# Performance work log

Hardware: AMD Instinct MI355X
Metric: run time of the kernel (lower is better)

## Reference

```python
import jax, jax.numpy as jnp
import numpy as np

N_E = 8192
E_DIM = 64
BETA = 0.25
DIVERSITY_GAMMA = 1.0
INV_TEMP = 100.0
EPS = 1e-05


def _entropy(p):
    # matches torch: (-p * log(clamp(p, min=eps))).sum(-1)
    return (-p * jnp.log(jnp.clip(p, EPS))).sum(axis=-1)


def setup_inputs() -> dict:
    key = jax.random.key(0)
    k1, k2 = jax.random.split(key)
    z = jax.random.normal(k1, (16, E_DIM, 32, 32), dtype=jnp.float32)
    # codebook, init like nn.Embedding then uniform_(-1/n_e, 1/n_e) scale doesn't matter for math;
    # use a small uniform init faithful to the module
    emb = jax.random.uniform(k2, (N_E, E_DIM), dtype=jnp.float32,
                             minval=-1.0 / N_E, maxval=1.0 / N_E)
    return {"z": z, "emb": emb}


def reference(z, emb):
    sg = jax.lax.stop_gradient
    # b c h w -> b h w c
    zp = jnp.transpose(z, (0, 2, 3, 1))            # [B,H,W,C]
    zf = zp.reshape(-1, E_DIM)                      # [N, C]
    # pairwise squared distances: ||z||^2 + ||e||^2 - 2 z e^T
    d = (jnp.sum(zf * zf, axis=1, keepdims=True)
         + jnp.sum(emb * emb, axis=1)
         - 2.0 * jnp.einsum('nd,kd->nk', zf, emb))  # [N, n_e]
    min_indices = jnp.argmin(d, axis=1)             # [N]
    z_q = emb[min_indices].reshape(zp.shape)        # gather, [B,H,W,C]
    # legacy commitment loss
    loss = (jnp.mean((sg(z_q) - zp) ** 2)
            + BETA * jnp.mean((z_q - sg(zp)) ** 2))
    # entropy aux loss (frac_per_sample_entropy == 1.0)
    prob = jax.nn.softmax(-d * INV_TEMP, axis=-1)   # [N, n_e]
    per_sample_entropy = _entropy(prob).mean()
    avg_prob = prob.mean(axis=0)                    # [n_e]
    codebook_entropy = _entropy(avg_prob)
    entropy_aux = per_sample_entropy - DIVERSITY_GAMMA * codebook_entropy
    # straight-through estimator
    z_q = zp + sg(z_q - zp)
    quantized = jnp.transpose(z_q, (0, 3, 1, 2))    # b h w c -> b c h w
    return quantized, loss, entropy_aux, min_indices
```

## Files before the change

kernel.cpp:

```cpp
#include <hip/hip_runtime.h>
#include <cfloat>


typedef __attribute__((ext_vector_type(8))) short short8v;
typedef __attribute__((ext_vector_type(4))) float f32x4;

#define C100L2E 144.26950408889634f
#define C200L2E 288.53900817779268f
#define LN2 0.6931471805599453

#define BLOB_TILE 33792
#define OFF_BLOB   0
#define OFF_INVZ   2162688
#define OFF_MINIDX 2228224
#define OFF_AVG    2293760
#define OFF_PSE    2326528
#define OFF_ZPART  2326544
#define OFF_S1PART (OFF_ZPART + 262144)
#define OFF_DMPART (OFF_S1PART + 262144)
#define OFF_IMPART (OFF_DMPART + 262144)
#define OFF_LOSSP  (OFF_IMPART + 262144)
#define OFF_ZZ     (OFF_LOSSP + 32768)

__device__ __forceinline__ unsigned short f2bf_rne(float f) {
    unsigned u = __float_as_uint(f);
    u = (u + 0x7fffu + ((u >> 16) & 1u)) >> 16;
    return (unsigned short)u;
}

__device__ __forceinline__ void gload_lds16(const void* g, void* l) {
    __builtin_amdgcn_global_load_lds(
        (const __attribute__((address_space(1))) unsigned int*)g,
        (__attribute__((address_space(3))) unsigned int*)l, 16, 0, 0);
}

__global__ __launch_bounds__(256) void k_prep(
    const float* __restrict__ emb, const float* __restrict__ z,
    char* __restrict__ blob, char* __restrict__ zblob, float* __restrict__ zz)
{
    if (blockIdx.x < 32) {
        const int k = blockIdx.x * 256 + threadIdx.x;
        const float* row = emb + k * 64;
        float fv[64];
#pragma unroll
        for (int i = 0; i < 16; ++i) {
            float4 v = ((const float4*)row)[i];
            fv[4 * i] = v.x; fv[4 * i + 1] = v.y; fv[4 * i + 2] = v.z; fv[4 * i + 3] = v.w;
        }
        float r8[8];
#pragma unroll
        for (int j = 0; j < 8; ++j) r8[j] = __fmul_rn(fv[j], fv[j]);
#pragma unroll
        for (int i = 8; i < 64; i += 8)
#pragma unroll
            for (int j = 0; j < 8; ++j)
                r8[j] = __fadd_rn(r8[j], __fmul_rn(fv[i + j], fv[i + j]));
        float s01 = __fadd_rn(r8[0], r8[1]), s23 = __fadd_rn(r8[2], r8[3]);
        float s45 = __fadd_rn(r8[4], r8[5]), s67 = __fadd_rn(r8[6], r8[7]);
        float e2 = __fadd_rn(__fadd_rn(s01, s23), __fadd_rn(s45, s67));

        char* tb = blob + (size_t)(k >> 7) * BLOB_TILE;
        const int r = k & 127;
        ((float*)(tb + 32768))[r] = e2;
        ((float*)(tb + 33280))[r] = e2 * C100L2E;
        const int sw = (r & 7) << 4;
#pragma unroll
        for (int dh = 0; dh < 2; ++dh)
#pragma unroll
            for (int cg = 0; cg < 4; ++cg) {
                short8v hv, lv;
#pragma unroll
                for (int e = 0; e < 8; ++e) {
                    float f = fv[dh * 32 + cg * 8 + e];
                    unsigned short hb = f2bf_rne(f);
                    float hf = __uint_as_float((unsigned)hb << 16);
                    hv[e] = (short)hb;
                    lv[e] = (short)f2bf_rne(f - hf);
                }
                const int byt = (r * 128 + dh * 64 + cg * 16) ^ sw;
                *(short8v*)(tb + byt) = hv;
                *(short8v*)(tb + 16384 + byt) = lv;
            }
    } else {
        const int r = (blockIdx.x - 32) * 256 + threadIdx.x;
        const float* src = z + (r >> 10) * 65536 + (r & 1023);
        float fv[64];
#pragma unroll
        for (int c = 0; c < 64; ++c) fv[c] = src[c * 1024];

        float r8[8];
#pragma unroll
        for (int j = 0; j < 8; ++j) r8[j] = __fmul_rn(fv[j], fv[j]);
#pragma unroll
        for (int i = 8; i < 64; i += 8)
#pragma unroll
            for (int j = 0; j < 8; ++j)
                r8[j] = __fadd_rn(r8[j], __fmul_rn(fv[i + j], fv[i + j]));
        float s01 = __fadd_rn(r8[0], r8[1]), s23 = __fadd_rn(r8[2], r8[3]);
        float s45 = __fadd_rn(r8[4], r8[5]), s67 = __fadd_rn(r8[6], r8[7]);
        zz[r] = __fadd_rn(__fadd_rn(s01, s23), __fadd_rn(s45, s67));

        char* tb = zblob + (size_t)(r >> 6) * 16384;
        const int rowp = r & 63;
#pragma unroll
        for (int cg = 0; cg < 8; ++cg) {
            short8v hv, lv;
#pragma unroll
            for (int e = 0; e < 8; ++e) {
                float f = fv[cg * 8 + e];
                unsigned short hb = f2bf_rne(f);
                float hf = __uint_as_float((unsigned)hb << 16);
                hv[e] = (short)hb;
                lv[e] = (short)f2bf_rne(f - hf);
            }
            *(short8v*)(tb + rowp * 128 + cg * 16) = hv;
            *(short8v*)(tb + 8192 + rowp * 128 + cg * 16) = lv;
        }
    }
}

#define STAGE_EMB(DSTBASE, TILE)                                                  \
    {                                                                             \
        const char* gsrc = blob + (size_t)(TILE) * BLOB_TILE;                     \
        char* ldst = (DSTBASE) + ((tid >> 6) << 10);                              \
        const char* g = gsrc + tid * 16;                                          \
        _Pragma("unroll")                                                         \
        for (int q = 0; q < 8; ++q)                                               \
            gload_lds16(g + q * 4096, ldst + q * 4096);                           \
        if (tid < 64) gload_lds16(gsrc + 32768 + (tid & 63) * 16,                 \
                                  (DSTBASE) + 32768);                             \
    }

#define STAGE512(DSTBASE, TILE)                                                   \
    {                                                                             \
        const char* gsrc = blob + (size_t)(TILE) * BLOB_TILE;                     \
        char* ldst = (DSTBASE) + ((tid >> 6) << 12);                              \
        const char* g = gsrc + ((tid >> 6) << 12) + (tid & 63) * 16;              \
        _Pragma("unroll")                                                         \
        for (int q = 0; q < 4; ++q)                                               \
            gload_lds16(g + q * 1024, ldst + q * 1024);                           \
        if (tid < 64) gload_lds16(gsrc + 32768 + (tid & 63) * 16,                 \
                                  (DSTBASE) + 32768);                             \
    }

__global__ __launch_bounds__(512) void k_pass1(
    const char* __restrict__ zblob, const char* __restrict__ blob,
    const float* __restrict__ zz,
    float* __restrict__ Zpart, float* __restrict__ S1part,
    float* __restrict__ dmpart, int* __restrict__ impart)
{
    __shared__ __align__(16) char smem[2 * BLOB_TILE];

    const int tid = threadIdx.x;
    const int panel = blockIdx.x >> 2;
    const int ks = blockIdx.x & 3;
    const int n0 = panel * 128;

    const int ln = tid & 63, wv = tid >> 6;
    const int lr = ln & 15, lg = ln >> 4;

    short8v Ah[2], Al[2];
    {
        const int p64 = (n0 >> 6) + (wv >> 2);
        const int rowp = (wv & 3) * 16 + lr;
        const char* tb = zblob + (size_t)p64 * 16384;
#pragma unroll
        for (int s = 0; s < 2; ++s) {
            const int byt = rowp * 128 + s * 64 + lg * 16;
            Ah[s] = *(const short8v*)(tb + byt);
            Al[s] = *(const short8v*)(tb + 8192 + byt);
        }
    }
    float zzr[4];
#pragma unroll
    for (int rg = 0; rg < 4; ++rg)
        zzr[rg] = zz[n0 + wv * 16 + lg * 4 + rg];

    STAGE512(smem, ks * 16);

    float Zp[4] = {0.f, 0.f, 0.f, 0.f}, S1p[4] = {0.f, 0.f, 0.f, 0.f};
    float dmin[4] = {FLT_MAX, FLT_MAX, FLT_MAX, FLT_MAX};
    int imin[4] = {0, 0, 0, 0};

    for (int it = 0; it < 16; ++it) {
        const int kbase = ks * 2048 + it * 128;
        __syncthreads();
        const char* bb = smem + (it & 1) * BLOB_TILE;
        if (it < 15) STAGE512(smem + ((it + 1) & 1) * BLOB_TILE, ks * 16 + it + 1);

        f32x4 acc[8];
#pragma unroll
        for (int f = 0; f < 8; ++f) { f32x4 zv = {0.f, 0.f, 0.f, 0.f}; acc[f] = zv; }

#pragma unroll
        for (int f = 0; f < 8; ++f) {
            const int rr = f * 16 + lr;
            const int sw2 = (rr & 7) << 4;
            short8v Bh[2], Bl[2];
#pragma unroll
            for (int s = 0; s < 2; ++s) {
                const int byt = (rr * 128 + s * 64 + lg * 16) ^ sw2;
                Bh[s] = *(const short8v*)(bb + byt);
                Bl[s] = *(const short8v*)(bb + 16384 + byt);
            }
#pragma unroll
            for (int s = 0; s < 2; ++s) {
                acc[f] = __builtin_amdgcn_mfma_f32_16x16x32_bf16(Ah[s], Bh[s], acc[f], 0, 0, 0);
                acc[f] = __builtin_amdgcn_mfma_f32_16x16x32_bf16(Ah[s], Bl[s], acc[f], 0, 0, 0);
                acc[f] = __builtin_amdgcn_mfma_f32_16x16x32_bf16(Al[s], Bh[s], acc[f], 0, 0, 0);
                acc[f] = __builtin_amdgcn_mfma_f32_16x16x32_bf16(Al[s], Bl[s], acc[f], 0, 0, 0);
            }
        }

#pragma unroll
        for (int f = 0; f < 8; ++f) {
            const float e2v = *(const float*)(bb + 32768 + (f * 16 + lr) * 4);
            const float c2 = *(const float*)(bb + 33280 + (f * 16 + lr) * 4);
            const int kk = kbase + f * 16 + lr;
#pragma unroll
            for (int rg = 0; rg < 4; ++rg) {
                const float sdot = acc[f][rg];
                const float t = fmaf(sdot, C200L2E, -c2);
                const float ex = __builtin_amdgcn_exp2f(t);
                Zp[rg] += ex;
                S1p[rg] = fmaf(t, ex, S1p[rg]);
                const float pre = __fadd_rn(zzr[rg], e2v);
                const float dnp = fmaf(-2.f, sdot, pre);
                if (dnp < dmin[rg]) { dmin[rg] = dnp; imin[rg] = kk; }
            }
        }
    }

#pragma unroll
    for (int msk = 1; msk < 16; msk <<= 1) {
#pragma unroll
        for (int rg = 0; rg < 4; ++rg) {
            float d2 = __shfl_xor(dmin[rg], msk, 16);
            int i2 = __shfl_xor(imin[rg], msk, 16);
            float Z2 = __shfl_xor(Zp[rg], msk, 16);
            float s2 = __shfl_xor(S1p[rg], msk, 16);
            if (d2 < dmin[rg] || (d2 == dmin[rg] && i2 < imin[rg])) {
                dmin[rg] = d2; imin[rg] = i2;
            }
            Zp[rg] += Z2;
            S1p[rg] += s2;
        }
    }
    if (lr == 0) {
#pragma unroll
        for (int rg = 0; rg < 4; ++rg) {
            const int n = n0 + wv * 16 + lg * 4 + rg;
            Zpart[ks * 16384 + n] = Zp[rg];
            S1part[ks * 16384 + n] = S1p[rg];
            dmpart[ks * 16384 + n] = dmin[rg];
            impart[ks * 16384 + n] = imin[rg];
        }
    }
}

__global__ __launch_bounds__(256) void k_rowred(
    const float* __restrict__ Zpart, const float* __restrict__ S1part,
    const float* __restrict__ dmpart, const int* __restrict__ impart,
    float* __restrict__ invZ, int* __restrict__ minidx,
    float* __restrict__ out_idx, double* __restrict__ pse_sum)
{
    const int n = blockIdx.x * 256 + threadIdx.x;
    float Z = __fadd_rn(__fadd_rn(Zpart[n], Zpart[16384 + n]),
                        __fadd_rn(Zpart[32768 + n], Zpart[49152 + n]));
    float S1 = __fadd_rn(__fadd_rn(S1part[n], S1part[16384 + n]),
                         __fadd_rn(S1part[32768 + n], S1part[49152 + n]));
    float dm = dmpart[n];
    int im = impart[n];
#pragma unroll
    for (int ksp = 1; ksp < 4; ++ksp) {
        float d2 = dmpart[ksp * 16384 + n];
        int i2 = impart[ksp * 16384 + n];
        if (d2 < dm || (d2 == dm && i2 < im)) { dm = d2; im = i2; }
    }
    minidx[n] = im;
    out_idx[n] = (float)im;
    float iz = 1.0f / Z;
    invZ[n] = iz;
    double h = log((double)Z) - LN2 * (double)S1 * (double)iz;
#pragma unroll
    for (int m = 32; m > 0; m >>= 1) h += __shfl_xor(h, m, 64);
    if ((threadIdx.x & 63) == 0) atomicAdd(pse_sum, h);
}

__global__ __launch_bounds__(256) void k_pass2(
    const char* __restrict__ zblob, const char* __restrict__ blob,
    const float* __restrict__ invZ, float* __restrict__ avg_acc)
{
    __shared__ __align__(16) char smem[BLOB_TILE + 4096];
    float* izAll = (float*)(smem + BLOB_TILE);

    const int tid = threadIdx.x;
    const int kt = blockIdx.x & 63;
    const int ns = blockIdx.x >> 6;
    const int ln = tid & 63, wv = tid >> 6;
    const int lr = ln & 15, lg = ln >> 4;

    STAGE_EMB(smem, kt);
    gload_lds16((const char*)(invZ + ns * 1024) + tid * 16,
                (char*)izAll + (wv << 10));
    __syncthreads();

    float c2v[8];
#pragma unroll
    for (int f = 0; f < 8; ++f)
        c2v[f] = *(const float*)(smem + 33280 + (f * 16 + lr) * 4);

    float acck[8] = {0.f, 0.f, 0.f, 0.f, 0.f, 0.f, 0.f, 0.f};

    for (int it = 0; it < 8; ++it) {
        short8v Ah[2][2], Al[2][2];
        const int p64 = ns * 16 + it * 2 + (wv >> 1);
        const char* tb = zblob + (size_t)p64 * 16384;
#pragma unroll
        for (int m = 0; m < 2; ++m) {
            const int rowp = (wv & 1) * 32 + m * 16 + lr;
#pragma unroll
            for (int s = 0; s < 2; ++s) {
                const int byt = rowp * 128 + s * 64 + lg * 16;
                Ah[m][s] = *(const short8v*)(tb + byt);
                Al[m][s] = *(const short8v*)(tb + 8192 + byt);
            }
        }
        const int izb = it * 128 + wv * 32 + lg * 4;
        float4 iz0 = *(const float4*)&izAll[izb];
        float4 iz1 = *(const float4*)&izAll[izb + 16];
        float izr[2][4] = {{iz0.x, iz0.y, iz0.z, iz0.w},
                           {iz1.x, iz1.y, iz1.z, iz1.w}};

#pragma unroll
        for (int fh = 0; fh < 2; ++fh) {
            f32x4 acc[2][4];
#pragma unroll
            for (int m = 0; m < 2; ++m)
#pragma unroll
                for (int fo = 0; fo < 4; ++fo) {
                    f32x4 zv = {0.f, 0.f, 0.f, 0.f};
                    acc[m][fo] = zv;
                }

#pragma unroll
            for (int fo = 0; fo < 4; ++fo) {
                const int f = fh * 4 + fo;
                const int rr = f * 16 + lr;
                const int sw2 = (rr & 7) << 4;
                short8v Bh[2], Bl[2];
#pragma unroll
                for (int s = 0; s < 2; ++s) {
                    const int byt = (rr * 128 + s * 64 + lg * 16) ^ sw2;
                    Bh[s] = *(const short8v*)(smem + byt);
                    Bl[s] = *(const short8v*)(smem + 16384 + byt);
                }
#pragma unroll
                for (int s = 0; s < 2; ++s)
#pragma unroll
                    for (int m = 0; m < 2; ++m) {
                        acc[m][fo] = __builtin_amdgcn_mfma_f32_16x16x32_bf16(Ah[m][s], Bh[s], acc[m][fo], 0, 0, 0);
                        acc[m][fo] = __builtin_amdgcn_mfma_f32_16x16x32_bf16(Ah[m][s], Bl[s], acc[m][fo], 0, 0, 0);
                        acc[m][fo] = __builtin_amdgcn_mfma_f32_16x16x32_bf16(Al[m][s], Bh[s], acc[m][fo], 0, 0, 0);
                    }
            }

#pragma unroll
            for (int fo = 0; fo < 4; ++fo) {
                const int f = fh * 4 + fo;
#pragma unroll
                for (int m = 0; m < 2; ++m)
#pragma unroll
                    for (int rg = 0; rg < 4; ++rg) {
                        const float t = fmaf(acc[m][fo][rg], C200L2E, -c2v[f]);
                        const float ex = __builtin_amdgcn_exp2f(t);
                        acck[f] = fmaf(ex, izr[m][rg], acck[f]);
                    }
            }
        }
    }

#pragma unroll
    for (int f = 0; f < 8; ++f) {
        float cs = acck[f];
        cs += __shfl_xor(cs, 16, 64);
        cs += __shfl_xor(cs, 32, 64);
        if (lg == 0) atomicAdd(&avg_acc[kt * 128 + f * 16 + lr], cs);
    }
}

__global__ __launch_bounds__(256) void k_quant(
    const float* __restrict__ z, const float* __restrict__ emb,
    const int* __restrict__ minidx, float* __restrict__ out,
    double* __restrict__ loss_part)
{
    __shared__ float lred[4];
    const int o4 = (blockIdx.x * 256 + threadIdx.x) * 4;
    const int nb = ((o4 >> 16) << 10) + (o4 & 1023);
    const int c = (o4 >> 10) & 63;
    const float4 zv = *(const float4*)(z + o4);
    const int i0 = minidx[nb], i1 = minidx[nb + 1];
    const int i2 = minidx[nb + 2], i3 = minidx[nb + 3];
    float4 ev;
    ev.x = emb[i0 * 64 + c];
    ev.y = emb[i1 * 64 + c];
    ev.z = emb[i2 * 64 + c];
    ev.w = emb[i3 * 64 + c];
    *(float4*)(out + o4) = ev;
    const float dx = ev.x - zv.x, dy = ev.y - zv.y;
    const float dz = ev.z - zv.z, dw = ev.w - zv.w;
    float sq = dx * dx + dy * dy + dz * dz + dw * dw;
#pragma unroll
    for (int m = 32; m > 0; m >>= 1) sq += __shfl_xor(sq, m, 64);
    if ((threadIdx.x & 63) == 0) lred[threadIdx.x >> 6] = sq;
    __syncthreads();
    if (threadIdx.x == 0)
        loss_part[blockIdx.x] = (double)lred[0] + (double)lred[1]
                              + (double)lred[2] + (double)lred[3];
}

__global__ __launch_bounds__(256) void k_final(
    const float* __restrict__ avg_acc, const double* __restrict__ pse_sum,
    const double* __restrict__ loss_part, float* __restrict__ out)
{
    __shared__ double red[256];
    const int tid = threadIdx.x;

    double lsum = 0.0;
    for (int k = tid; k < 1024; k += 256) lsum += loss_part[k];
    red[tid] = lsum;
    __syncthreads();
    for (int s = 128; s > 0; s >>= 1) {
        if (tid < s) red[tid] += red[tid + s];
        __syncthreads();
    }
    double ltot = red[0];
    __syncthreads();

    double local = 0.0;
    for (int k = tid; k < 8192; k += 256) {
        float p = avg_acc[k] * (1.0f / 16384.0f);
        float cl = fmaxf(p, 1e-5f);
        local += (double)(-p * logf(cl));
    }
    red[tid] = local;
    __syncthreads();
    for (int s = 128; s > 0; s >>= 1) {
        if (tid < s) red[tid] += red[tid + s];
        __syncthreads();
    }
    if (tid == 0) {
        double ce = red[0];
        double pse = pse_sum[0] / 16384.0;
        out[1048576] = (float)(1.25 * ltot / 1048576.0);
        out[1048577] = (float)(pse - ce);
    }
}

extern "C" void kernel_launch(void* const* d_in, const int* in_sizes, int n_in,
                              void* d_out, int out_size, void* d_ws, size_t ws_size,
                              hipStream_t stream) {
    const float* z = (const float*)d_in[0];
    const float* emb = (const float*)d_in[1];
    float* out = (float*)d_out;
    char* ws = (char*)d_ws;
    char* blob = ws + OFF_BLOB;
    float* invZ = (float*)(ws + OFF_INVZ);
    int* minidx = (int*)(ws + OFF_MINIDX);
    float* avg_acc = (float*)(ws + OFF_AVG);
    double* pse_sum = (double*)(ws + OFF_PSE);
    float* Zpart = (float*)(ws + OFF_ZPART);
    float* S1part = (float*)(ws + OFF_S1PART);
    float* dmpart = (float*)(ws + OFF_DMPART);
    int* impart = (int*)(ws + OFF_IMPART);
    double* loss_part = (double*)(ws + OFF_LOSSP);
    float* zz = (float*)(ws + OFF_ZZ);
    char* zblob = (char*)d_out;

    hipMemsetAsync(ws + OFF_AVG, 0, 32768 + 16, stream);

    k_prep<<<96, 256, 0, stream>>>(emb, z, blob, zblob, zz);
    k_pass1<<<512, 512, 0, stream>>>(zblob, blob, zz, Zpart, S1part, dmpart, impart);
    k_rowred<<<64, 256, 0, stream>>>(Zpart, S1part, dmpart, impart,
                                     invZ, minidx, out + 1048578, pse_sum);
    k_pass2<<<1024, 256, 0, stream>>>(zblob, blob, invZ, avg_acc);
    k_quant<<<1024, 256, 0, stream>>>(z, emb, minidx, out, loss_part);
    k_final<<<1, 256, 0, stream>>>(avg_acc, pse_sum, loss_part, out);
}
```

Measured before the change: 192.2 us.

## Restructure pass2 to stream codebook tiles with double-buffered LDS per row panel

The codebook-probability pass now has each 512-thread block own a 128-row panel of z held in registers and a quarter of the codebook. The block streams 16 codebook tiles through double-buffered LDS, so tile loads overlap the MFMA and exp work. Per-code sums are reduced first into an LDS accumulator with shared atomics, then written to global with one atomic per entry. This replaces re-reading z for every codebook tile and the single-buffered staging, at the cost of a barrier per tile, more LDS, and LDS atomics inside the loop.

```diff
diff --git a/kernel.cpp b/kernel.cpp
--- a/kernel.cpp
+++ b/kernel.cpp
@@ -119,18 +119,6 @@
     }
 }
 
-#define STAGE_EMB(DSTBASE, TILE)                                                  \
-    {                                                                             \
-        const char* gsrc = blob + (size_t)(TILE) * BLOB_TILE;                     \
-        char* ldst = (DSTBASE) + ((tid >> 6) << 10);                              \
-        const char* g = gsrc + tid * 16;                                          \
-        _Pragma("unroll")                                                         \
-        for (int q = 0; q < 8; ++q)                                               \
-            gload_lds16(g + q * 4096, ldst + q * 4096);                           \
-        if (tid < 64) gload_lds16(gsrc + 32768 + (tid & 63) * 16,                 \
-                                  (DSTBASE) + 32768);                             \
-    }
-
 #define STAGE512(DSTBASE, TILE)                                                   \
     {                                                                             \
         const char* gsrc = blob + (size_t)(TILE) * BLOB_TILE;                     \
@@ -287,106 +275,91 @@
     if ((threadIdx.x & 63) == 0) atomicAdd(pse_sum, h);
 }
 
-__global__ __launch_bounds__(256) void k_pass2(
+__global__ __launch_bounds__(512) void k_pass2(
     const char* __restrict__ zblob, const char* __restrict__ blob,
     const float* __restrict__ invZ, float* __restrict__ avg_acc)
 {
-    __shared__ __align__(16) char smem[BLOB_TILE + 4096];
-    float* izAll = (float*)(smem + BLOB_TILE);
+    __shared__ __align__(16) char smem[2 * BLOB_TILE + 8192];
+    float* avgL = (float*)(smem + 2 * BLOB_TILE);
 
     const int tid = threadIdx.x;
-    const int kt = blockIdx.x & 63;
-    const int ns = blockIdx.x >> 6;
+    const int panel = blockIdx.x >> 2;
+    const int ks = blockIdx.x & 3;
+    const int n0 = panel * 128;
+
     const int ln = tid & 63, wv = tid >> 6;
     const int lr = ln & 15, lg = ln >> 4;
 
-    STAGE_EMB(smem, kt);
-    gload_lds16((const char*)(invZ + ns * 1024) + tid * 16,
-                (char*)izAll + (wv << 10));
+    short8v Ah[2], Al[2];
+    {
+        const int p64 = (n0 >> 6) + (wv >> 2);
+        const int rowp = (wv & 3) * 16 + lr;
+        const char* tb = zblob + (size_t)p64 * 16384;
+#pragma unroll
+        for (int s = 0; s < 2; ++s) {
+            const int byt = rowp * 128 + s * 64 + lg * 16;
+            Ah[s] = *(const short8v*)(tb + byt);
+            Al[s] = *(const short8v*)(tb + 8192 + byt);
+        }
+    }
+    float izr[4];
+#pragma unroll
+    for (int rg = 0; rg < 4; ++rg)
+        izr[rg] = invZ[n0 + wv * 16 + lg * 4 + rg];
+
+#pragma unroll
+    for (int i = 0; i < 4; ++i) avgL[tid * 4 + i] = 0.f;
+
+    STAGE512(smem, ks * 16);
+
+    for (int it = 0; it < 16; ++it) {
+        __syncthreads();
+        const char* bb = smem + (it & 1) * BLOB_TILE;
+        if (it < 15) STAGE512(smem + ((it + 1) & 1) * BLOB_TILE, ks * 16 + it + 1);
+
+        f32x4 acc[8];
+#pragma unroll
+        for (int f = 0; f < 8; ++f) { f32x4 zv = {0.f, 0.f, 0.f, 0.f}; acc[f] = zv; }
+
+#pragma unroll
+        for (int f = 0; f < 8; ++f) {
+            const int rr = f * 16 + lr;
+            const int sw2 = (rr & 7) << 4;
+            short8v Bh[2], Bl[2];
+#pragma unroll
+            for (int s = 0; s < 2; ++s) {
+                const int byt = (rr * 128 + s * 64 + lg * 16) ^ sw2;
+                Bh[s] = *(const short8v*)(bb + byt);
+                Bl[s] = *(const short8v*)(bb + 16384 + byt);
+            }
+#pragma unroll
+            for (int s = 0; s < 2; ++s) {
+                acc[f] = __builtin_amdgcn_mfma_f32_16x16x32_bf16(Ah[s], Bh[s], acc[f], 0, 0, 0);
+                acc[f] = __builtin_amdgcn_mfma_f32_16x16x32_bf16(Ah[s], Bl[s], acc[f], 0, 0, 0);
+                acc[f] = __builtin_amdgcn_mfma_f32_16x16x32_bf16(Al[s], Bh[s], acc[f], 0, 0, 0);
+            }
+        }
+
+#pragma unroll
+        for (int f = 0; f < 8; ++f) {
+            const float c2 = *(const float*)(bb + 33280 + (f * 16 + lr) * 4);
+            float cs = 0.f;
+#pragma unroll
+            for (int rg = 0; rg < 4; ++rg) {
+                const float t = fmaf(acc[f][rg], C200L2E, -c2);
+                const float ex = __builtin_amdgcn_exp2f(t);
+                cs = fmaf(ex, izr[rg], cs);
+            }
+            cs += __shfl_xor(cs, 16, 64);
+            cs += __shfl_xor(cs, 32, 64);
+            if (lg == 0) atomicAdd(&avgL[it * 128 + f * 16 + lr], cs);
+        }
+    }
+
     __syncthreads();
-
-    float c2v[8];
-#pragma unroll
-    for (int f = 0; f < 8; ++f)
-        c2v[f] = *(const float*)(smem + 33280 + (f * 16 + lr) * 4);
-
-    float acck[8] = {0.f, 0.f, 0.f, 0.f, 0.f, 0.f, 0.f, 0.f};
-
-    for (int it = 0; it < 8; ++it) {
-        short8v Ah[2][2], Al[2][2];
-        const int p64 = ns * 16 + it * 2 + (wv >> 1);
-        const char* tb = zblob + (size_t)p64 * 16384;
-#pragma unroll
-        for (int m = 0; m < 2; ++m) {
-            const int rowp = (wv & 1) * 32 + m * 16 + lr;
-#pragma unroll
-            for (int s = 0; s < 2; ++s) {
-                const int byt = rowp * 128 + s * 64 + lg * 16;
-                Ah[m][s] = *(const short8v*)(tb + byt);
-                Al[m][s] = *(const short8v*)(tb + 8192 + byt);
-            }
-        }
-        const int izb = it * 128 + wv * 32 + lg * 4;
-        float4 iz0 = *(const float4*)&izAll[izb];
-        float4 iz1 = *(const float4*)&izAll[izb + 16];
-        float izr[2][4] = {{iz0.x, iz0.y, iz0.z, iz0.w},
-                           {iz1.x, iz1.y, iz1.z, iz1.w}};
-
-#pragma unroll
-        for (int fh = 0; fh < 2; ++fh) {
-            f32x4 acc[2][4];
-#pragma unroll
-            for (int m = 0; m < 2; ++m)
-#pragma unroll
-                for (int fo = 0; fo < 4; ++fo) {
-                    f32x4 zv = {0.f, 0.f, 0.f, 0.f};
-                    acc[m][fo] = zv;
-                }
-
-#pragma unroll
-            for (int fo = 0; fo < 4; ++fo) {
-                const int f = fh * 4 + fo;
-                const int rr = f * 16 + lr;
-                const int sw2 = (rr & 7) << 4;
-                short8v Bh[2], Bl[2];
-#pragma unroll
-                for (int s = 0; s < 2; ++s) {
-                    const int byt = (rr * 128 + s * 64 + lg * 16) ^ sw2;
-                    Bh[s] = *(const short8v*)(smem + byt);
-                    Bl[s] = *(const short8v*)(smem + 16384 + byt);
-                }
-#pragma unroll
-                for (int s = 0; s < 2; ++s)
-#pragma unroll
-                    for (int m = 0; m < 2; ++m) {
-                        acc[m][fo] = __builtin_amdgcn_mfma_f32_16x16x32_bf16(Ah[m][s], Bh[s], acc[m][fo], 0, 0, 0);
-                        acc[m][fo] = __builtin_amdgcn_mfma_f32_16x16x32_bf16(Ah[m][s], Bl[s], acc[m][fo], 0, 0, 0);
-                        acc[m][fo] = __builtin_amdgcn_mfma_f32_16x16x32_bf16(Al[m][s], Bh[s], acc[m][fo], 0, 0, 0);
-                    }
-            }
-
-#pragma unroll
-            for (int fo = 0; fo < 4; ++fo) {
-                const int f = fh * 4 + fo;
-#pragma unroll
-                for (int m = 0; m < 2; ++m)
-#pragma unroll
-                    for (int rg = 0; rg < 4; ++rg) {
-                        const float t = fmaf(acc[m][fo][rg], C200L2E, -c2v[f]);
-                        const float ex = __builtin_amdgcn_exp2f(t);
-                        acck[f] = fmaf(ex, izr[m][rg], acck[f]);
-                    }
-            }
-        }
-    }
-
-#pragma unroll
-    for (int f = 0; f < 8; ++f) {
-        float cs = acck[f];
-        cs += __shfl_xor(cs, 16, 64);
-        cs += __shfl_xor(cs, 32, 64);
-        if (lg == 0) atomicAdd(&avg_acc[kt * 128 + f * 16 + lr], cs);
-    }
+#pragma unroll
+    for (int i = 0; i < 4; ++i)
+        atomicAdd(&avg_acc[ks * 2048 + tid * 4 + i], avgL[tid * 4 + i]);
 }
 
 __global__ __launch_bounds__(256) void k_quant(
@@ -483,7 +456,7 @@
     k_pass1<<<512, 512, 0, stream>>>(zblob, blob, zz, Zpart, S1part, dmpart, impart);
     k_rowred<<<64, 256, 0, stream>>>(Zpart, S1part, dmpart, impart,
                                      invZ, minidx, out + 1048578, pse_sum);
-    k_pass2<<<1024, 256, 0, stream>>>(zblob, blob, invZ, avg_acc);
+    k_pass2<<<512, 512, 0, stream>>>(zblob, blob, invZ, avg_acc);
     k_quant<<<1024, 256, 0, stream>>>(z, emb, minidx, out, loss_part);
     k_final<<<1, 256, 0, stream>>>(avg_acc, pse_sum, loss_part, out);
 }
```

After: 208.5 us. +8.5%, slower.
